# Performance work log

Hardware: AMD Instinct MI355X
Metric: run time of the kernel (lower is better)

The kernel has to match this reference:

```python
import jax, jax.numpy as jnp
import numpy as np

N = 262144   # batch of states
D = 32       # in_dim

def setup_inputs() -> dict:
    key = jax.random.key(0)
    k1, k2 = jax.random.split(key)
    x = jax.random.normal(k1, (N, D), dtype=jnp.float32)
    # learned bilinear tensor W[k, i, j], as in nn.Parameter(Tensor(D, D, D))
    weight = jax.random.normal(k2, (D, D, D), dtype=jnp.float32) * (1.0 / np.sqrt(D))
    return {"x": x, "weight": weight}

def reference(x, weight):
    # torch: xBx = x @ W @ x.T -> (D, N, N); out = diagonal(xBx.permute(2,1,0)).t()
    # i.e. out[n, k] = sum_{i,j} x[n,i] * W[k,i,j] * x[n,j]
    # Compute the batched quadratic form directly, skipping the (D, N, N) tensor.
    xW = jnp.einsum('ni,kij->nkj', x, weight)   # (N, D, D) intermediate
    out = jnp.einsum('nkj,nj->nk', xW, x)       # (N, D)
    return out
```

## Files before the change

kernel.cpp:

```cpp
#include <hip/hip_runtime.h>


typedef _Float16 f16x2 __attribute__((ext_vector_type(2)));
typedef _Float16 f16x4 __attribute__((ext_vector_type(4)));
typedef _Float16 f16x8 __attribute__((ext_vector_type(8)));
typedef float    f32x16 __attribute__((ext_vector_type(16)));

static __device__ __forceinline__ unsigned int pk2_f16(float lo, float hi) {
    return __builtin_bit_cast(unsigned int, __builtin_amdgcn_cvt_pkrtz(lo, hi));
}
static __device__ __forceinline__ f16x2 u2h(unsigned int u) {
    return __builtin_bit_cast(f16x2, u);
}
static __device__ __forceinline__ unsigned short f16b(float f) {
    _Float16 h = (_Float16)f;
    return __builtin_bit_cast(unsigned short, h);
}

__global__ __launch_bounds__(256)
void prep_btab_sym(const float* __restrict__ W, unsigned short* __restrict__ bt) {
    __shared__ float Wlds[1024];
    const int k = blockIdx.x;
    const int t = threadIdx.x;
    {
        const float4* src = (const float4*)(W + k * 1024);
        ((float4*)Wlds)[t] = src[t];
    }
    __syncthreads();
    if (t < 66) {
        int n  = t >> 1;
        int lh = t & 1;
        int d  = (n == 32) ? 16 : (n >> 1);
        int q  = (n == 32) ? 0  : (n & 1);
        unsigned short v[8];
        #pragma unroll
        for (int b = 0; b < 8; ++b) {
            int i = q * 16 + lh * 8 + b;
            int j = (i + d) & 31;
            float s = (d == 0) ? Wlds[i * 32 + i]
                               : Wlds[i * 32 + j] + Wlds[j * 32 + i];
            v[b] = f16b(s);
        }
        uint4 pk;
        pk.x = (unsigned int)v[0] | ((unsigned int)v[1] << 16);
        pk.y = (unsigned int)v[2] | ((unsigned int)v[3] << 16);
        pk.z = (unsigned int)v[4] | ((unsigned int)v[5] << 16);
        pk.w = (unsigned int)v[6] | ((unsigned int)v[7] << 16);
        ((uint4*)bt)[n * 64 + k + lh * 32] = pk;
    }
}

__global__ __launch_bounds__(512, 8)
void quadform_kernel(const float* __restrict__ x,
                     const unsigned short* __restrict__ bt_ws,
                     float* __restrict__ out) {
    __shared__ __align__(16) unsigned short btab[33 * 64 * 8];

    const int tid  = threadIdx.x;
    const int lane = tid & 63;
    const int wave = tid >> 6;
    const int hi   = lane >> 5;
    const int rl   = lane & 31;
    const long wrow = (long)blockIdx.x * 256 + wave * 32;

    const float4* xr = (const float4*)(x + (wrow + rl) * 32);

    {
        const uint4* src = (const uint4*)bt_ws;
        uint4* dst = (uint4*)btab;
        #pragma unroll
        for (int c = 0; c < 5; ++c) {
            int idx = c * 512 + tid;
            if (idx < 2112) dst[idx] = src[idx];
        }
    }

    unsigned int ypk[16];
    {
        unsigned int xpk[16];
        #pragma unroll
        for (int c = 0; c < 8; ++c) {
            float4 v = xr[c];
            xpk[2 * c + 0] = pk2_f16(v.x, v.y);
            xpk[2 * c + 1] = pk2_f16(v.z, v.w);
        }
        #pragma unroll
        for (int c = 0; c < 16; ++c)
            ypk[c] = hi ? xpk[(c + 4) & 15] : xpk[c];
    }

    f32x16 acc;
    #pragma unroll
    for (int e = 0; e < 16; ++e) acc[e] = 0.0f;

    __syncthreads();

    #pragma unroll
    for (int s = 0; s < 33; ++s) {
        const int d   = (s == 32) ? 16 : (s >> 1);
        const int q8  = ((s == 32) ? 0 : (s & 1)) * 8;
        const int dh  = d >> 1;
        const bool od = (d & 1) != 0;
        f16x8 bfrag = *(const f16x8*)(&btab[(s * 64 + lane) * 8]);

        f16x2 b0 = od ? u2h(__builtin_amdgcn_perm(ypk[(q8 + 0 + dh + 1) & 15], ypk[(q8 + 0 + dh) & 15], 0x05040302u)) : u2h(ypk[(q8 + 0 + dh) & 15]);
        f16x2 b1 = od ? u2h(__builtin_amdgcn_perm(ypk[(q8 + 1 + dh + 1) & 15], ypk[(q8 + 1 + dh) & 15], 0x05040302u)) : u2h(ypk[(q8 + 1 + dh) & 15]);
        f16x2 b2 = od ? u2h(__builtin_amdgcn_perm(ypk[(q8 + 2 + dh + 1) & 15], ypk[(q8 + 2 + dh) & 15], 0x05040302u)) : u2h(ypk[(q8 + 2 + dh) & 15]);
        f16x2 b3 = od ? u2h(__builtin_amdgcn_perm(ypk[(q8 + 3 + dh + 1) & 15], ypk[(q8 + 3 + dh) & 15], 0x05040302u)) : u2h(ypk[(q8 + 3 + dh) & 15]);
        f16x2 a0 = u2h(ypk[q8 + 0]) * b0;
        f16x2 a1 = u2h(ypk[q8 + 1]) * b1;
        f16x2 a2 = u2h(ypk[q8 + 2]) * b2;
        f16x2 a3 = u2h(ypk[q8 + 3]) * b3;
        f16x4 lo = __builtin_shufflevector(a0, a1, 0, 1, 2, 3);
        f16x4 hf = __builtin_shufflevector(a2, a3, 0, 1, 2, 3);
        f16x8 a  = __builtin_shufflevector(lo, hf, 0, 1, 2, 3, 4, 5, 6, 7);
        acc = __builtin_amdgcn_mfma_f32_32x32x16_f16(a, bfrag, acc, 0, 0, 0);
    }

    float* ob = out + (wrow + 4 * hi) * 32 + rl;
    #pragma unroll
    for (int e = 0; e < 16; ++e)
        __builtin_nontemporal_store(acc[e], ob + (e & 3) * 32 + (e >> 2) * 256);
}

extern "C" void kernel_launch(void* const* d_in, const int* in_sizes, int n_in,
                              void* d_out, int out_size, void* d_ws, size_t ws_size,
                              hipStream_t stream) {
    const float* x = (const float*)d_in[0];
    const float* W = (const float*)d_in[1];
    float* out = (float*)d_out;
    unsigned short* bt = (unsigned short*)d_ws;

    prep_btab_sym<<<32, 256, 0, stream>>>(W, bt);
    int nrows = in_sizes[0] / 32;
    int grid  = nrows / 256;
    quadform_kernel<<<grid, 512, 0, stream>>>(x, bt, out);
}
```

Baseline: 26.75 us.

## Coalesce x loads through LDS staging and double block size

Each block now covers 512 rows with 1024 threads. It loads x with fully coalesced float4 reads, converts to fp16 and stages it in padded LDS, and issues the btab copy as register loads before the LDS stores. Before, each lane read its own 128-byte row with strided float4 loads. The intent is better global-memory coalescing and amortizing the btab load over twice as many rows. The cost is roughly 75KB of LDS per block, which limits occupancy, plus an extra LDS round trip.

```diff
diff --git a/kernel.cpp b/kernel.cpp
--- a/kernel.cpp
+++ b/kernel.cpp
@@ -50,39 +50,65 @@
     }
 }
 
-__global__ __launch_bounds__(512, 8)
+#define XS 20
+
+__global__ __launch_bounds__(1024, 8)
 void quadform_kernel(const float* __restrict__ x,
                      const unsigned short* __restrict__ bt_ws,
                      float* __restrict__ out) {
     __shared__ __align__(16) unsigned short btab[33 * 64 * 8];
+    __shared__ __align__(16) unsigned int   xstage[512 * XS];
 
     const int tid  = threadIdx.x;
     const int lane = tid & 63;
     const int wave = tid >> 6;
     const int hi   = lane >> 5;
     const int rl   = lane & 31;
-    const long wrow = (long)blockIdx.x * 256 + wave * 32;
+    const long blockrow = (long)blockIdx.x * 512;
+    const long wrow = blockrow + wave * 32;
 
-    const float4* xr = (const float4*)(x + (wrow + rl) * 32);
+    const float4* xsrc = (const float4*)(x + blockrow * 32);
+    float4 xg0 = xsrc[tid];
+    float4 xg1 = xsrc[1024 + tid];
+    float4 xg2 = xsrc[2048 + tid];
+    float4 xg3 = xsrc[3072 + tid];
 
+    const uint4* bsrc = (const uint4*)bt_ws;
+    uint4 b0 = bsrc[tid];
+    uint4 b1 = bsrc[1024 + tid];
+    uint4 b2;
+    if (tid < 64) b2 = bsrc[2048 + tid];
+
+    #pragma unroll
+    for (int c = 0; c < 4; ++c) {
+        float4 v = (c == 0) ? xg0 : (c == 1) ? xg1 : (c == 2) ? xg2 : xg3;
+        int idx = c * 1024 + tid;
+        int row = idx >> 3;
+        int sub = idx & 7;
+        uint2 w2;
+        w2.x = pk2_f16(v.x, v.y);
+        w2.y = pk2_f16(v.z, v.w);
+        *(uint2*)&xstage[row * XS + sub * 2] = w2;
+    }
     {
-        const uint4* src = (const uint4*)bt_ws;
         uint4* dst = (uint4*)btab;
-        #pragma unroll
-        for (int c = 0; c < 5; ++c) {
-            int idx = c * 512 + tid;
-            if (idx < 2112) dst[idx] = src[idx];
-        }
+        dst[tid]        = b0;
+        dst[1024 + tid] = b1;
+        if (tid < 64) dst[2048 + tid] = b2;
     }
+    __syncthreads();
 
     unsigned int ypk[16];
     {
         unsigned int xpk[16];
+        const unsigned int* xr = &xstage[(wave * 32 + rl) * XS];
         #pragma unroll
-        for (int c = 0; c < 8; ++c) {
-            float4 v = xr[c];
-            xpk[2 * c + 0] = pk2_f16(v.x, v.y);
-            xpk[2 * c + 1] = pk2_f16(v.z, v.w);
+        for (int c = 0; c < 4; ++c) {
+            uint4 v = *(const uint4*)(xr + c * 4);
+            xpk[c * 4 + 0] = v.x;
+            xpk[c * 4 + 1] = v.y;
+            xpk[c * 4 + 2] = v.z;
+            xpk[c * 4 + 3] = v.w;
         }
         #pragma unroll
         for (int c = 0; c < 16; ++c)
@@ -92,8 +118,6 @@
     f32x16 acc;
     #pragma unroll
     for (int e = 0; e < 16; ++e) acc[e] = 0.0f;
-
-    __syncthreads();
 
     #pragma unroll
     for (int s = 0; s < 33; ++s) {
@@ -133,6 +157,6 @@
 
     prep_btab_sym<<<32, 256, 0, stream>>>(W, bt);
     int nrows = in_sizes[0] / 32;
-    int grid  = nrows / 256;
-    quadform_kernel<<<grid, 512, 0, stream>>>(x, bt, out);
+    int grid  = nrows / 512;
+    quadform_kernel<<<grid, 1024, 0, stream>>>(x, bt, out);
 }
```

New measurement: 22.75 us (median of 2 runs). 14.9% less time.

## Stage x via coalesced loads into LDS, read B table from global

Applied to the files above, without the earlier changes.

Each wave now loads its 32 rows of x with fully coalesced float4 loads, converts them to packed f16, and stages them in a padded per-wave LDS buffer before each lane reads back its own row. The B-table is no longer copied into shared memory; every MFMA step loads its fragment straight from global/L2. This also removes the block-wide __syncthreads. The intent is to cut the strided per-row global loads and the table-copy-plus-barrier cost, at the risk of 33 dependent global loads per wave in the main loop.

```diff
diff --git a/kernel.cpp b/kernel.cpp
--- a/kernel.cpp
+++ b/kernel.cpp
@@ -50,11 +50,13 @@
     }
 }
 
+#define XS 18
+
 __global__ __launch_bounds__(512, 8)
 void quadform_kernel(const float* __restrict__ x,
-                     const unsigned short* __restrict__ bt_ws,
+                     const uint4* __restrict__ bt,
                      float* __restrict__ out) {
-    __shared__ __align__(16) unsigned short btab[33 * 64 * 8];
+    __shared__ __align__(16) unsigned int xstage[256 * XS];
 
     const int tid  = threadIdx.x;
     const int lane = tid & 63;
@@ -63,26 +65,36 @@
     const int rl   = lane & 31;
     const long wrow = (long)blockIdx.x * 256 + wave * 32;
 
-    const float4* xr = (const float4*)(x + (wrow + rl) * 32);
+    const float4* xsrc = (const float4*)(x + wrow * 32);
+    float4 v0 = xsrc[lane];
+    float4 v1 = xsrc[64 + lane];
+    float4 v2 = xsrc[128 + lane];
+    float4 v3 = xsrc[192 + lane];
 
-    {
-        const uint4* src = (const uint4*)bt_ws;
-        uint4* dst = (uint4*)btab;
-        #pragma unroll
-        for (int c = 0; c < 5; ++c) {
-            int idx = c * 512 + tid;
-            if (idx < 2112) dst[idx] = src[idx];
-        }
+    unsigned int* ws = &xstage[wave * 32 * XS];
+    #pragma unroll
+    for (int c = 0; c < 4; ++c) {
+        float4 v = (c == 0) ? v0 : (c == 1) ? v1 : (c == 2) ? v2 : v3;
+        int idx = c * 64 + lane;
+        int row = idx >> 3;
+        int sub = idx & 7;
+        uint2 w2;
+        w2.x = pk2_f16(v.x, v.y);
+        w2.y = pk2_f16(v.z, v.w);
+        *(uint2*)&ws[row * XS + sub * 2] = w2;
     }
 
     unsigned int ypk[16];
     {
         unsigned int xpk[16];
+        const unsigned int* xr = &ws[rl * XS];
         #pragma unroll
-        for (int c = 0; c < 8; ++c) {
-            float4 v = xr[c];
-            xpk[2 * c + 0] = pk2_f16(v.x, v.y);
-            xpk[2 * c + 1] = pk2_f16(v.z, v.w);
+        for (int c = 0; c < 4; ++c) {
+            uint4 v = *(const uint4*)(xr + c * 4);
+            xpk[c * 4 + 0] = v.x;
+            xpk[c * 4 + 1] = v.y;
+            xpk[c * 4 + 2] = v.z;
+            xpk[c * 4 + 3] = v.w;
         }
         #pragma unroll
         for (int c = 0; c < 16; ++c)
@@ -93,15 +105,14 @@
     #pragma unroll
     for (int e = 0; e < 16; ++e) acc[e] = 0.0f;
 
-    __syncthreads();
-
     #pragma unroll
     for (int s = 0; s < 33; ++s) {
         const int d   = (s == 32) ? 16 : (s >> 1);
         const int q8  = ((s == 32) ? 0 : (s & 1)) * 8;
         const int dh  = d >> 1;
         const bool od = (d & 1) != 0;
-        f16x8 bfrag = *(const f16x8*)(&btab[(s * 64 + lane) * 8]);
+        uint4 bu = bt[s * 64 + lane];
+        f16x8 bfrag = __builtin_bit_cast(f16x8, bu);
 
         f16x2 b0 = od ? u2h(__builtin_amdgcn_perm(ypk[(q8 + 0 + dh + 1) & 15], ypk[(q8 + 0 + dh) & 15], 0x05040302u)) : u2h(ypk[(q8 + 0 + dh) & 15]);
         f16x2 b1 = od ? u2h(__builtin_amdgcn_perm(ypk[(q8 + 1 + dh + 1) & 15], ypk[(q8 + 1 + dh) & 15], 0x05040302u)) : u2h(ypk[(q8 + 1 + dh) & 15]);
@@ -134,5 +145,5 @@
     prep_btab_sym<<<32, 256, 0, stream>>>(W, bt);
     int nrows = in_sizes[0] / 32;
     int grid  = nrows / 256;
-    quadform_kernel<<<grid, 512, 0, stream>>>(x, bt, out);
+    quadform_kernel<<<grid, 512, 0, stream>>>(x, (const uint4*)bt, out);
 }
```

New measurement: 31.23 us. 1.17x slower.
